# Performance work log

Hardware: AMD Instinct MI355X
Metric: run time of the kernel (lower is better)

The kernel has to match this reference:

```python
import jax, jax.numpy as jnp
import numpy as np

# dims matching init_kwargs
B, N = 1, 2048
VOCAB, DIM, DEPTH = 32000, 1024, 4
HEADS, DIM_HEAD, WINDOW = 16, 64, 512
INNER = HEADS * DIM_HEAD          # 1024
FF_INNER = int(DIM * 4 * 2 / 3)   # 2730 (GEGLU inner)
DPB_DIM = DIM // 2
LN_EPS = 1e-5


def layernorm(x, g, b):
    m = jnp.mean(x, axis=-1, keepdims=True)
    v = jnp.mean(jnp.square(x - m), axis=-1, keepdims=True)
    return (x - m) * jax.lax.rsqrt(v + LN_EPS) * g + b


def look_around(x, backward=1, forward=0, pad_value=-1):
    # x: [b, nw, w, ...]; concat shifted windows along the window_size axis
    nw = x.shape[1]
    pads = [(0, 0), (backward, forward)] + [(0, 0)] * (x.ndim - 2)
    px = jnp.pad(x, pads, constant_values=pad_value)
    return jnp.concatenate([px[:, i:i + nw] for i in range(backward + forward + 1)], axis=2)


def dynamic_pos_bias(w1, b1, w2, b2, w3, b3, i, j):
    # MLP over scalar relative distances, then gather into [H, i, j]
    rel = jnp.arange(j, dtype=jnp.float32)[:, None]            # [j, 1]
    h = jax.nn.silu(rel @ w1 + b1)
    h = jax.nn.silu(h @ w2 + b2)
    bias = h @ w3 + b3                                          # [j, H]
    idx = jnp.abs(jnp.arange(j - i, j)[:, None] - jnp.arange(j)[None, :])  # [i, j]
    return jnp.transpose(bias[idx], (2, 0, 1))                  # [H, i, j]


def local_attention(q, k, v, attn_bias):
    # causal sliding-window attention, look_backward=1, look_forward=0, exact_windowsize=True
    # q,k,v: [B,H,N,dh]; N assumed multiple of WINDOW (autopad is a no-op then)
    b, h, n, d = q.shape
    w = WINDOW
    nw = n // w
    scale = d ** -0.5
    bq = q.reshape(b * h, nw, w, d) * scale
    bk = look_around(k.reshape(b * h, nw, w, d), pad_value=-1.0)   # [bh,nw,2w,d]
    bv = look_around(v.reshape(b * h, nw, w, d), pad_value=-1.0)
    t = jnp.arange(n).reshape(1, nw, w)
    bq_t = t[..., :, None]                                      # [1,nw,w,1]
    bq_k = look_around(t, pad_value=-1)[..., None, :]           # [1,nw,1,2w]
    # causal | exact-window | padding masks
    mask = (bq_t < bq_k) | (bq_t > bq_k + w) | (bq_k == -1)
    sim = jnp.einsum('bwid,bwjd->bwij', bq, bk)                 # [bh,nw,w,2w]
    sim = (sim.reshape(b, h, nw, w, 2 * w) + attn_bias[None, :, None]).reshape(b * h, nw, w, 2 * w)
    sim = jnp.where(mask, -jnp.finfo(sim.dtype).max, sim)
    attn = jax.nn.softmax(sim, axis=-1)
    out = jnp.einsum('bwij,bwjd->bwid', attn, bv)
    return out.reshape(b, h, n, d)


def forward(tokens, tok_emb, pos_emb, dpb_w1, dpb_b1, dpb_w2, dpb_b2, dpb_w3, dpb_b3,
            ln1_g, ln1_b, Wqkv, Wo, ln2_g, ln2_b, Wff1, Wff2, lnf_g, lnf_b, Wlogits):
    bsz, n = tokens.shape
    x = tok_emb[tokens] + pos_emb[:n]                           # [B,N,D]
    bias = dynamic_pos_bias(dpb_w1, dpb_b1, dpb_w2, dpb_b2, dpb_w3, dpb_b3, WINDOW, 2 * WINDOW)

    def split_heads(t):
        return t.reshape(bsz, n, HEADS, DIM_HEAD).transpose(0, 2, 1, 3)

    for l in range(DEPTH):
        # LocalMHA (prenorm) + residual
        h = layernorm(x, ln1_g[l], ln1_b[l])
        q, k, v = jnp.split(h @ Wqkv[l], 3, axis=-1)
        o = local_attention(split_heads(q), split_heads(k), split_heads(v), bias)
        o = o.transpose(0, 2, 1, 3).reshape(bsz, n, INNER)
        x = x + o @ Wo[l]
        # GEGLU FFN (prenorm inside FeedForward) + residual
        h = layernorm(x, ln2_g[l], ln2_b[l])
        a, gate = jnp.split(h @ Wff1[l], 2, axis=-1)
        x = x + (a * jax.nn.gelu(gate, approximate=False)) @ Wff2[l]

    return layernorm(x, lnf_g, lnf_b) @ Wlogits                 # [B,N,V]


def setup_inputs() -> dict:
    key = jax.random.key(0)
    ks = iter(jax.random.split(key, 16))
    s = 0.02
    rn = lambda *shape: jax.random.normal(next(ks), shape, dtype=jnp.float32) * s
    return {
        'tokens': jax.random.randint(next(ks), (B, N), 0, VOCAB, dtype=jnp.int32),
        'tok_emb': rn(VOCAB, DIM),
        'pos_emb': rn(N, DIM),
        'dpb_w1': rn(1, DPB_DIM), 'dpb_b1': jnp.zeros((DPB_DIM,), jnp.float32),
        'dpb_w2': rn(DPB_DIM, DPB_DIM), 'dpb_b2': jnp.zeros((DPB_DIM,), jnp.float32),
        'dpb_w3': rn(DPB_DIM, HEADS), 'dpb_b3': jnp.zeros((HEADS,), jnp.float32),
        'ln1_g': jnp.ones((DEPTH, DIM), jnp.float32), 'ln1_b': jnp.zeros((DEPTH, DIM), jnp.float32),
        'Wqkv': rn(DEPTH, DIM, 3 * INNER),
        'Wo': rn(DEPTH, INNER, DIM),
        'ln2_g': jnp.ones((DEPTH, DIM), jnp.float32), 'ln2_b': jnp.zeros((DEPTH, DIM), jnp.float32),
        'Wff1': rn(DEPTH, DIM, 2 * FF_INNER),
        'Wff2': rn(DEPTH, FF_INNER, DIM),
        'lnf_g': jnp.ones((DIM,), jnp.float32), 'lnf_b': jnp.zeros((DIM,), jnp.float32),
        'Wlogits': rn(DIM, VOCAB),
    }


def reference(tokens, tok_emb, pos_emb, dpb_w1, dpb_b1, dpb_w2, dpb_b2, dpb_w3, dpb_b3,
              ln1_g, ln1_b, Wqkv, Wo, ln2_g, ln2_b, Wff1, Wff2, lnf_g, lnf_b, Wlogits):
    return forward(tokens, tok_emb, pos_emb, dpb_w1, dpb_b1, dpb_w2, dpb_b2, dpb_w3, dpb_b3,
                   ln1_g, ln1_b, Wqkv, Wo, ln2_g, ln2_b, Wff1, Wff2, lnf_g, lnf_b, Wlogits)
```

## Files before the change

### kernel.cpp

```cpp
#include <hip/hip_runtime.h>
#include <cstdint>

#define DEV __device__ __forceinline__

typedef __attribute__((ext_vector_type(8))) short bf16x8;
typedef __attribute__((ext_vector_type(4))) short bf16x4;
typedef __attribute__((ext_vector_type(4))) float f32x4;
typedef __attribute__((ext_vector_type(8))) unsigned short u16x8;

DEV float bf2f(unsigned short u) { return __uint_as_float(((unsigned)u) << 16); }
DEV unsigned short f2bf(float f) {
  unsigned u = __float_as_uint(f);
  u += 0x7FFFu + ((u >> 16) & 1u);
  return (unsigned short)(u >> 16);
}

DEV void gload_lds16(const void* g, void* lds) {
  __builtin_amdgcn_global_load_lds(
      (const __attribute__((address_space(1))) unsigned int*)g,
      (__attribute__((address_space(3))) unsigned int*)lds, 16, 0, 0);
}

__global__ __launch_bounds__(256) void k_prep(
    const int* __restrict__ tokens, const float* __restrict__ tok_emb,
    const float* __restrict__ pos_emb, float* __restrict__ x,
    const float* __restrict__ w1, const float* __restrict__ b1,
    const float* __restrict__ w2, const float* __restrict__ b2,
    const float* __restrict__ w3, const float* __restrict__ b3,
    float* __restrict__ table,
    const float* __restrict__ Wqkv, unsigned short* __restrict__ WqkvT,
    const float* __restrict__ Wo, unsigned short* __restrict__ WoT,
    const float* __restrict__ Wff1, unsigned short* __restrict__ Wff1T,
    const float* __restrict__ Wff2, unsigned short* __restrict__ Wff2T,
    const float* __restrict__ Wlog, unsigned short* __restrict__ WlogT) {
  __shared__ float smem[64 * 65];
  int b = blockIdx.x, t = threadIdx.x;
  if (b < 2048) {
    int tok = tokens[b];
    int c = t * 4;
    float4 a = *(const float4*)(tok_emb + (long)tok * 1024 + c);
    float4 p = *(const float4*)(pos_emb + (long)b * 1024 + c);
    float4 r;
    r.x = a.x + p.x; r.y = a.y + p.y; r.z = a.z + p.z; r.w = a.w + p.w;
    *(float4*)(x + (long)b * 1024 + c) = r;
    return;
  }
  b -= 2048;
  if (b < 1024) {
    float* h1 = smem;
    float* h2 = smem + 512;
    float rf = (float)b;
    for (int c = t; c < 512; c += 256) {
      float v = rf * w1[c] + b1[c];
      h1[c] = v / (1.0f + __expf(-v));
    }
    __syncthreads();
    for (int c = t; c < 512; c += 256) {
      float acc = b2[c];
      for (int k2 = 0; k2 < 512; ++k2) acc = fmaf(h1[k2], w2[(long)k2 * 512 + c], acc);
      h2[c] = acc / (1.0f + __expf(-acc));
    }
    __syncthreads();
    if (t < 16) {
      float acc = b3[t];
      for (int k2 = 0; k2 < 512; ++k2) acc = fmaf(h2[k2], w3[k2 * 16 + t], acc);
      table[b * 16 + t] = acc;
    }
    return;
  }
  b -= 1024;
  const float* src; unsigned short* dst;
  int K, N, Kp, nx, ny, mode;
  long ss, ds;
  if (b < 3072) {
    src = Wqkv; dst = WqkvT; K = 1024; N = 3072; Kp = 1024;
    nx = 48; ny = 16; mode = 0; ss = 1024L * 3072; ds = 3072L * 1024;
  } else if ((b -= 3072) < 1024) {
    src = Wo; dst = WoT; K = 1024; N = 1024; Kp = 1024;
    nx = 16; ny = 16; mode = 0; ss = 1024L * 1024; ds = 1024L * 1024;
  } else if ((b -= 1024) < 5504) {
    src = Wff1; dst = Wff1T; K = 1024; N = 5460; Kp = 1024;
    nx = 86; ny = 16; mode = 1; ss = 1024L * 5460; ds = 5504L * 1024;
  } else if ((b -= 5504) < 2752) {
    src = Wff2; dst = Wff2T; K = 2730; N = 1024; Kp = 2752;
    nx = 16; ny = 43; mode = 0; ss = 2730L * 1024; ds = 1024L * 2752;
  } else {
    b -= 2752;
    src = Wlog; dst = WlogT; K = 1024; N = 32000; Kp = 1024;
    nx = 500; ny = 16; mode = 0; ss = 0; ds = 0;
  }
  int z = b / (nx * ny);
  int rem = b % (nx * ny);
  int n0 = (rem % nx) * 64, k0 = (rem / nx) * 64;
  src += (long)z * ss;
  dst += (long)z * ds;
  float (*tile)[65] = (float(*)[65])smem;
  const int cr = t >> 4, cc = (t & 15) * 4;
#pragma unroll
  for (int i = 0; i < 4; ++i) {
    int kr = cr + 16 * i;
    int k = k0 + kr, n = n0 + cc;
    float4 v = make_float4(0.f, 0.f, 0.f, 0.f);
    if (k < K && n < N) v = *(const float4*)(src + (long)k * N + n);
    tile[kr][cc + 0] = v.x;
    tile[kr][cc + 1] = v.y;
    tile[kr][cc + 2] = v.z;
    tile[kr][cc + 3] = v.w;
  }
  __syncthreads();
  const int kc = (t & 7) * 8;
#pragma unroll
  for (int it = 0; it < 2; ++it) {
    int nr = (t >> 3) + 32 * it;
    u16x8 o;
#pragma unroll
    for (int e = 0; e < 8; ++e) o[e] = f2bf(tile[kc + e][nr]);
    int nrow = n0 + nr;
    if (mode)
      nrow = nrow < 2730 ? 2 * nrow : (nrow < 5460 ? 2 * (nrow - 2730) + 1 : nrow);
    *(u16x8*)(dst + (long)nrow * Kp + k0 + kc) = o;
  }
}

__global__ __launch_bounds__(256) void k_ln4(const float* __restrict__ x,
    const float* __restrict__ g, const float* __restrict__ b,
    unsigned short* __restrict__ out) {
  const int row = blockIdx.x * 4 + (threadIdx.x >> 6);
  const int l = threadIdx.x & 63;
  const float* xr = x + (long)row * 1024 + l * 16;
  float4 v[4];
#pragma unroll
  for (int e = 0; e < 4; ++e) v[e] = ((const float4*)xr)[e];
  float s = 0.0f;
#pragma unroll
  for (int e = 0; e < 4; ++e) s += v[e].x + v[e].y + v[e].z + v[e].w;
#pragma unroll
  for (int off = 32; off; off >>= 1) s += __shfl_xor(s, off);
  float mean = s * (1.0f / 1024.0f);
  float sq = 0.0f;
#pragma unroll
  for (int e = 0; e < 4; ++e) {
    float a0 = v[e].x - mean, a1 = v[e].y - mean, a2 = v[e].z - mean, a3 = v[e].w - mean;
    sq += a0 * a0 + a1 * a1 + a2 * a2 + a3 * a3;
  }
#pragma unroll
  for (int off = 32; off; off >>= 1) sq += __shfl_xor(sq, off);
  float inv = rsqrtf(sq * (1.0f / 1024.0f) + 1e-5f);
  const float* gr = g + l * 16;
  const float* br = b + l * 16;
  unsigned short* orow = out + (long)row * 1024 + l * 16;
#pragma unroll
  for (int e = 0; e < 4; ++e) {
    float4 gv = ((const float4*)gr)[e];
    float4 bv = ((const float4*)br)[e];
    ushort4 o;
    o.x = f2bf((v[e].x - mean) * inv * gv.x + bv.x);
    o.y = f2bf((v[e].y - mean) * inv * gv.y + bv.y);
    o.z = f2bf((v[e].z - mean) * inv * gv.z + bv.z);
    o.w = f2bf((v[e].w - mean) * inv * gv.w + bv.w);
    ((ushort4*)orow)[e] = o;
  }
}

__global__ __launch_bounds__(256, 2) void k_attn_mfma(
    const unsigned short* __restrict__ qkv, const float* __restrict__ table,
    unsigned short* __restrict__ o) {
  __shared__ unsigned short Ks[64 * 64];
  __shared__ unsigned short Vt[64 * 72];
  __shared__ unsigned short Ps[4][16 * 72];
  __shared__ float biasl[1024];
  const int qt = blockIdx.x, h = blockIdx.y, wi = blockIdx.z;
  const int iw0 = qt * 64;
  const int t = threadIdx.x;
  const int w = t >> 6, l = t & 63;
  const int lq = l & 15, lk = l >> 4;

  for (int i = t; i < 1024; i += 256) biasl[i] = table[i * 16 + h];

  const unsigned short* qp = qkv + (long)(wi * 512 + iw0 + w * 16 + lq) * 3072 + h * 64;
  bf16x8 qf0 = *(const bf16x8*)(qp + lk * 8);
  bf16x8 qf1 = *(const bf16x8*)(qp + 32 + lk * 8);

  f32x4 oacc[4] = {};
  float mrun[4] = {-3.0e38f, -3.0e38f, -3.0e38f, -3.0e38f};
  float srun[4] = {};

  const int kt0 = (wi == 0) ? 8 : qt;
  const int kt1 = qt + 8;
  for (int kt = kt0; kt <= kt1; ++kt) {
    const int ktbase = kt * 64;
    const long kgbase = (long)((wi - 1) * 512 + ktbase);
    __syncthreads();
    {
      const unsigned short* Kg = qkv + kgbase * 3072 + 1024 + h * 64;
#pragma unroll
      for (int s2 = 0; s2 < 2; ++s2) {
        int g = s2 * 4 + w;
        int row = g * 8 + (l >> 3);
        int gch = (l & 7) ^ (row & 7);
        gload_lds16(Kg + (long)row * 3072 + gch * 8, &Ks[g * 512]);
      }
    }
    {
      int kp = t & 31, dg = t >> 5;
      const unsigned short* Vg =
          qkv + (kgbase + 2 * kp) * 3072 + 2048 + h * 64 + dg * 8;
      bf16x8 a0 = *(const bf16x8*)Vg;
      bf16x8 a1 = *(const bf16x8*)(Vg + 3072);
#pragma unroll
      for (int e = 0; e < 8; ++e) {
        unsigned pack = ((unsigned)(unsigned short)a0[e]) |
                        (((unsigned)(unsigned short)a1[e]) << 16);
        *(unsigned*)&Vt[(dg * 8 + e) * 72 + 2 * kp] = pack;
      }
    }
    asm volatile("s_waitcnt vmcnt(0)" ::: "memory");
    __syncthreads();

    f32x4 sacc[4] = {};
#pragma unroll
    for (int ct = 0; ct < 4; ++ct) {
      int krow = ct * 16 + lq;
      bf16x8 kf0 = *(const bf16x8*)&Ks[krow * 64 + (((0 + lk) ^ (krow & 7)) * 8)];
      bf16x8 kf1 = *(const bf16x8*)&Ks[krow * 64 + (((4 + lk) ^ (krow & 7)) * 8)];
      sacc[ct] = __builtin_amdgcn_mfma_f32_16x16x32_bf16(qf0, kf0, sacc[ct], 0, 0, 0);
      sacc[ct] = __builtin_amdgcn_mfma_f32_16x16x32_bf16(qf1, kf1, sacc[ct], 0, 0, 0);
    }

#pragma unroll
    for (int r = 0; r < 4; ++r) {
      const int iw = iw0 + w * 16 + lk * 4 + r;
      float sc[4];
#pragma unroll
      for (int ct = 0; ct < 4; ++ct) {
        int jj = ktbase + ct * 16 + lq;
        int di = 512 + iw - jj;
        int dic = min(max(di, 0), 1023);
        bool allowed = (jj >= iw) && (jj <= iw + 512);
        float v = sacc[ct][r] * 0.125f + biasl[dic];
        sc[ct] = allowed ? v : -3.0e38f;
      }
      float mx = fmaxf(fmaxf(sc[0], sc[1]), fmaxf(sc[2], sc[3]));
      mx = fmaxf(mx, __shfl_xor(mx, 1));
      mx = fmaxf(mx, __shfl_xor(mx, 2));
      mx = fmaxf(mx, __shfl_xor(mx, 4));
      mx = fmaxf(mx, __shfl_xor(mx, 8));
      float mnew = fmaxf(mrun[r], mx);
      float f = __expf(mrun[r] - mnew);
      mrun[r] = mnew;
      float rs = 0.0f;
#pragma unroll
      for (int ct = 0; ct < 4; ++ct) {
        float pv = __expf(sc[ct] - mnew);
        rs += pv;
        Ps[w][(lk * 4 + r) * 72 + ct * 16 + lq] = f2bf(pv);
      }
      rs += __shfl_xor(rs, 1);
      rs += __shfl_xor(rs, 2);
      rs += __shfl_xor(rs, 4);
      rs += __shfl_xor(rs, 8);
      srun[r] = srun[r] * f + rs;
#pragma unroll
      for (int dt = 0; dt < 4; ++dt) oacc[dt][r] *= f;
    }
    asm volatile("s_waitcnt lgkmcnt(0)" ::: "memory");

#pragma unroll
    for (int ks = 0; ks < 2; ++ks) {
      bf16x4 pa0 = *(const bf16x4*)&Ps[w][lq * 72 + ks * 32 + lk * 8];
      bf16x4 pa1 = *(const bf16x4*)&Ps[w][lq * 72 + ks * 32 + lk * 8 + 4];
      bf16x8 pa = __builtin_shufflevector(pa0, pa1, 0, 1, 2, 3, 4, 5, 6, 7);
#pragma unroll
      for (int dt = 0; dt < 4; ++dt) {
        int drow = dt * 16 + lq;
        bf16x4 vb0 = *(const bf16x4*)&Vt[drow * 72 + ks * 32 + lk * 8];
        bf16x4 vb1 = *(const bf16x4*)&Vt[drow * 72 + ks * 32 + lk * 8 + 4];
        bf16x8 vb = __builtin_shufflevector(vb0, vb1, 0, 1, 2, 3, 4, 5, 6, 7);
        oacc[dt] = __builtin_amdgcn_mfma_f32_16x16x32_bf16(pa, vb, oacc[dt], 0, 0, 0);
      }
    }
  }

  unsigned short* ob =
      o + (long)(wi * 512 + iw0 + w * 16 + lk * 4) * 1024 + h * 64 + lq;
#pragma unroll
  for (int r = 0; r < 4; ++r) {
    float inv = 1.0f / srun[r];
#pragma unroll
    for (int dt = 0; dt < 4; ++dt)
      ob[(long)r * 1024 + dt * 16] = f2bf(oacc[dt][r] * inv);
  }
}

template <int EPI, int BM>
__global__ __launch_bounds__(256, 2) void k_gemm(const unsigned short* __restrict__ A,
    const unsigned short* __restrict__ BT, void* __restrict__ Cout,
    int N, int K, int nbm) {
  constexpr int MI = BM / 32;
  __shared__ unsigned short As[BM * 64];
  __shared__ unsigned short Bs[128 * 64];
  const int nwg = gridDim.x;
  const int orig = blockIdx.x;
  const int q8 = nwg >> 3, r8 = nwg & 7;
  const int xcd = orig & 7, i8 = orig >> 3;
  const int wgid = (xcd < r8 ? xcd * (q8 + 1) : r8 * (q8 + 1) + (xcd - r8) * q8) + i8;
  const int bm = wgid % nbm;
  const int bn = wgid / nbm;
  const int t = threadIdx.x;
  const int w = t >> 6, l = t & 63;
  const int wm = w >> 1, wn = w & 1;
  const int lrow = l >> 3, lch = l & 7;
  const int lq = l & 15, lk = l >> 4;
  f32x4 acc[MI][4] = {};
  const long arow0 = (long)bm * BM, brow0 = (long)bn * 128;
  for (int kt = 0; kt < K; kt += 64) {
    __syncthreads();
#pragma unroll
    for (int s2 = 0; s2 < 4; ++s2) {
      int grp = s2 * 4 + w;
      int r = grp * 8 + lrow;
      int gch = lch ^ lrow;
      gload_lds16(BT + (brow0 + r) * K + kt + gch * 8, &Bs[grp * 512]);
      if (s2 < MI)
        gload_lds16(A + (arow0 + r) * K + kt + gch * 8, &As[grp * 512]);
    }
    asm volatile("s_waitcnt vmcnt(0)" ::: "memory");
    __syncthreads();
#pragma unroll
    for (int kk = 0; kk < 2; ++kk) {
      bf16x8 af[MI], bfr[4];
#pragma unroll
      for (int i = 0; i < MI; ++i) {
        int ra = wm * (BM / 2) + i * 16 + lq;
        af[i] = *(const bf16x8*)&As[ra * 64 + (((kk * 4 + lk) ^ (ra & 7)) * 8)];
      }
#pragma unroll
      for (int j = 0; j < 4; ++j) {
        int rb = wn * 64 + j * 16 + lq;
        bfr[j] = *(const bf16x8*)&Bs[rb * 64 + (((kk * 4 + lk) ^ (rb & 7)) * 8)];
      }
#pragma unroll
      for (int i = 0; i < MI; ++i)
#pragma unroll
        for (int j = 0; j < 4; ++j)
          acc[i][j] = __builtin_amdgcn_mfma_f32_16x16x32_bf16(af[i], bfr[j],
                                                              acc[i][j], 0, 0, 0);
    }
  }
  const int rbase = bm * BM + wm * (BM / 2) + lk * 4;
  const int cbase = bn * 128 + wn * 64 + lq;
#pragma unroll
  for (int i = 0; i < MI; ++i) {
#pragma unroll
    for (int j = 0; j < 4; ++j) {
#pragma unroll
      for (int r2 = 0; r2 < 4; ++r2) {
        long row = rbase + i * 16 + r2;
        long col = cbase + j * 16;
        float v = acc[i][j][r2];
        if (EPI == 0) {
          ((unsigned short*)Cout)[row * N + col] = f2bf(v);
        } else if (EPI == 1) {
          ((float*)Cout)[row * N + col] += v;
        } else if (EPI == 2) {
          ((float*)Cout)[row * N + col] = v;
        } else {
          float gpart = __shfl_xor(v, 1);
          if ((lq & 1) == 0) {
            float uval =
                v * (0.5f * gpart * (1.0f + erff(gpart * 0.70710678118654752f)));
            ((unsigned short*)Cout)[row * (N >> 1) + (col >> 1)] = f2bf(uval);
          }
        }
      }
    }
  }
}

extern "C" void kernel_launch(void* const* d_in, const int* in_sizes, int n_in,
                              void* d_out, int out_size, void* d_ws, size_t ws_size,
                              hipStream_t stream) {
  (void)in_sizes; (void)n_in; (void)out_size; (void)ws_size;
  const int* tokens   = (const int*)d_in[0];
  const float* tok_emb = (const float*)d_in[1];
  const float* pos_emb = (const float*)d_in[2];
  const float* dpb_w1 = (const float*)d_in[3];
  const float* dpb_b1 = (const float*)d_in[4];
  const float* dpb_w2 = (const float*)d_in[5];
  const float* dpb_b2 = (const float*)d_in[6];
  const float* dpb_w3 = (const float*)d_in[7];
  const float* dpb_b3 = (const float*)d_in[8];
  const float* ln1_g  = (const float*)d_in[9];
  const float* ln1_b  = (const float*)d_in[10];
  const float* Wqkv   = (const float*)d_in[11];
  const float* Wo     = (const float*)d_in[12];
  const float* ln2_g  = (const float*)d_in[13];
  const float* ln2_b  = (const float*)d_in[14];
  const float* Wff1   = (const float*)d_in[15];
  const float* Wff2   = (const float*)d_in[16];
  const float* lnf_g  = (const float*)d_in[17];
  const float* lnf_b  = (const float*)d_in[18];
  const float* Wlog   = (const float*)d_in[19];
  float* out = (float*)d_out;

  char* p = (char*)d_ws;
  auto carve = [&](size_t bytes) {
    char* q = p;
    p += (bytes + 255) & ~(size_t)255;
    return (void*)q;
  };
  unsigned short* WqkvT = (unsigned short*)carve((size_t)4 * 3072 * 1024 * 2);
  unsigned short* WoT   = (unsigned short*)carve((size_t)4 * 1024 * 1024 * 2);
  unsigned short* Wff1T = (unsigned short*)carve((size_t)4 * 5504 * 1024 * 2);
  unsigned short* Wff2T = (unsigned short*)carve((size_t)4 * 1024 * 2752 * 2);
  unsigned short* WlogT = (unsigned short*)carve((size_t)32000 * 1024 * 2);
  float*          x     = (float*)carve((size_t)2048 * 1024 * 4);
  unsigned short* hbuf  = (unsigned short*)carve((size_t)2048 * 1024 * 2);
  unsigned short* qkv   = (unsigned short*)carve((size_t)2048 * 3072 * 2);
  unsigned short* ao    = (unsigned short*)carve((size_t)2048 * 1024 * 2);
  unsigned short* ubuf  = (unsigned short*)carve((size_t)2048 * 2752 * 2);
  float*          table = (float*)carve((size_t)1024 * 16 * 4);

  k_prep<<<23424, 256, 0, stream>>>(
      tokens, tok_emb, pos_emb, x, dpb_w1, dpb_b1, dpb_w2, dpb_b2, dpb_w3,
      dpb_b3, table, Wqkv, WqkvT, Wo, WoT, Wff1, Wff1T, Wff2, Wff2T, Wlog, WlogT);

  for (int l = 0; l < 4; ++l) {
    k_ln4<<<512, 256, 0, stream>>>(x, ln1_g + l * 1024, ln1_b + l * 1024, hbuf);
    k_gemm<0, 128><<<dim3(16 * (3072 / 128)), 256, 0, stream>>>(
        hbuf, WqkvT + (long)l * 3072 * 1024, qkv, 3072, 1024, 16);
    k_attn_mfma<<<dim3(8, 16, 4), 256, 0, stream>>>(qkv, table, ao);
    k_gemm<1, 64><<<dim3(32 * (1024 / 128)), 256, 0, stream>>>(
        ao, WoT + (long)l * 1024 * 1024, x, 1024, 1024, 32);
    k_ln4<<<512, 256, 0, stream>>>(x, ln2_g + l * 1024, ln2_b + l * 1024, hbuf);
    k_gemm<3, 128><<<dim3(16 * (5504 / 128)), 256, 0, stream>>>(
        hbuf, Wff1T + (long)l * 5504 * 1024, ubuf, 5504, 1024, 16);
    k_gemm<1, 64><<<dim3(32 * (1024 / 128)), 256, 0, stream>>>(
        ubuf, Wff2T + (long)l * 1024 * 2752, x, 1024, 2752, 32);
  }
  k_ln4<<<512, 256, 0, stream>>>(x, lnf_g, lnf_b, hbuf);
  k_gemm<2, 128><<<dim3(16 * (32000 / 128)), 256, 0, stream>>>(
      hbuf, WlogT, out, 32000, 1024, 16);
}
```

Baseline: 1.047 ms.

## Pre-tile weights into swizzled 128x64 blocks so GEMM B-loads are contiguous

The weight conversion kernel now writes each transposed bf16 weight as contiguous 128-row by 64-k tiles, already XOR-swizzled to match the LDS layout. The GEMM B-operand load then becomes one linear 16-byte-per-lane copy per tile, with no per-row strided addressing. Prep blocks now cover 128x64 tiles, which halves the prep grid, and the GEGLU interleave is handled by a separate gather path. The cost is a more complex prep kernel with a larger shared tile, plus reliance on every GEMM N being a multiple of 128.

Result: slower. 1.072 ms (+2.4%).

```diff
diff --git a/kernel.cpp b/kernel.cpp
--- a/kernel.cpp
+++ b/kernel.cpp
@@ -33,7 +33,7 @@
     const float* __restrict__ Wff1, unsigned short* __restrict__ Wff1T,
     const float* __restrict__ Wff2, unsigned short* __restrict__ Wff2T,
     const float* __restrict__ Wlog, unsigned short* __restrict__ WlogT) {
-  __shared__ float smem[64 * 65];
+  __shared__ float smem[64 * 132];
   int b = blockIdx.x, t = threadIdx.x;
   if (b < 2048) {
     int tok = tokens[b];
@@ -70,55 +70,100 @@
   }
   b -= 1024;
   const float* src; unsigned short* dst;
-  int K, N, Kp, nx, ny, mode;
-  long ss, ds;
-  if (b < 3072) {
-    src = Wqkv; dst = WqkvT; K = 1024; N = 3072; Kp = 1024;
-    nx = 48; ny = 16; mode = 0; ss = 1024L * 3072; ds = 3072L * 1024;
-  } else if ((b -= 3072) < 1024) {
-    src = Wo; dst = WoT; K = 1024; N = 1024; Kp = 1024;
-    nx = 16; ny = 16; mode = 0; ss = 1024L * 1024; ds = 1024L * 1024;
-  } else if ((b -= 1024) < 5504) {
-    src = Wff1; dst = Wff1T; K = 1024; N = 5460; Kp = 1024;
-    nx = 86; ny = 16; mode = 1; ss = 1024L * 5460; ds = 5504L * 1024;
-  } else if ((b -= 5504) < 2752) {
-    src = Wff2; dst = Wff2T; K = 2730; N = 1024; Kp = 2752;
-    nx = 16; ny = 43; mode = 0; ss = 2730L * 1024; ds = 1024L * 2752;
+  int N, Kreal, nt, kt, mode;
+  if (b < 1536) {
+    int z = b / 384, r = b % 384;
+    nt = r / 16; kt = r % 16; mode = 0; N = 3072; Kreal = 1024;
+    src = Wqkv + (long)z * 1024 * 3072;
+    dst = WqkvT + ((long)z * 384 + r) * 8192;
+  } else if ((b -= 1536) < 512) {
+    int z = b / 128, r = b % 128;
+    nt = r / 16; kt = r % 16; mode = 0; N = 1024; Kreal = 1024;
+    src = Wo + (long)z * 1024 * 1024;
+    dst = WoT + ((long)z * 128 + r) * 8192;
+  } else if ((b -= 512) < 2752) {
+    int z = b / 688, r = b % 688;
+    nt = r / 16; kt = r % 16; mode = 1; N = 5460; Kreal = 1024;
+    src = Wff1 + (long)z * 1024 * 5460;
+    dst = Wff1T + ((long)z * 688 + r) * 8192;
+  } else if ((b -= 2752) < 1376) {
+    int z = b / 344, r = b % 344;
+    nt = r / 43; kt = r % 43; mode = 0; N = 1024; Kreal = 2730;
+    src = Wff2 + (long)z * 2730 * 1024;
+    dst = Wff2T + ((long)z * 344 + r) * 8192;
   } else {
-    b -= 2752;
-    src = Wlog; dst = WlogT; K = 1024; N = 32000; Kp = 1024;
-    nx = 500; ny = 16; mode = 0; ss = 0; ds = 0;
-  }
-  int z = b / (nx * ny);
-  int rem = b % (nx * ny);
-  int n0 = (rem % nx) * 64, k0 = (rem / nx) * 64;
-  src += (long)z * ss;
-  dst += (long)z * ds;
-  float (*tile)[65] = (float(*)[65])smem;
-  const int cr = t >> 4, cc = (t & 15) * 4;
-#pragma unroll
-  for (int i = 0; i < 4; ++i) {
-    int kr = cr + 16 * i;
-    int k = k0 + kr, n = n0 + cc;
-    float4 v = make_float4(0.f, 0.f, 0.f, 0.f);
-    if (k < K && n < N) v = *(const float4*)(src + (long)k * N + n);
-    tile[kr][cc + 0] = v.x;
-    tile[kr][cc + 1] = v.y;
-    tile[kr][cc + 2] = v.z;
-    tile[kr][cc + 3] = v.w;
+    b -= 1376;
+    nt = b / 16; kt = b % 16; mode = 0; N = 32000; Kreal = 1024;
+    src = Wlog;
+    dst = WlogT + (long)b * 8192;
+  }
+  const int k0 = kt * 64;
+  float (*tf)[132] = (float(*)[132])smem;
+  if (mode == 0) {
+    const int nb = nt * 128 + (t & 15) * 8;
+#pragma unroll
+    for (int ii = 0; ii < 4; ++ii) {
+      int row = (t >> 4) + 16 * ii;
+      int k = k0 + row;
+      float4 v0 = {0.f, 0.f, 0.f, 0.f}, v1 = v0;
+      if (k < Kreal) {
+        const float* sp = src + (long)k * N + nb;
+        v0 = *(const float4*)sp;
+        v1 = *(const float4*)(sp + 4);
+      }
+      int cs = (t & 15) * 8;
+      *(float4*)&tf[row][cs] = v0;
+      *(float4*)&tf[row][cs + 4] = v1;
+    }
+  } else {
+    const int row = t >> 2;
+    const int k = k0 + row;
+    const int fo = (t & 3) * 16;
+    const int fb = nt * 64;
+    const float* sr = src + (long)k * 5460;
+#pragma unroll
+    for (int j = 0; j < 4; ++j) {
+      int f = fb + fo + 4 * j;
+      float4 av;
+      if (f + 3 < 2730) {
+        av = *(const float4*)(sr + f);
+      } else {
+        av.x = (f < 2730) ? sr[f] : 0.f;
+        av.y = (f + 1 < 2730) ? sr[f + 1] : 0.f;
+        av.z = (f + 2 < 2730) ? sr[f + 2] : 0.f;
+        av.w = 0.f;
+      }
+      int lc = 2 * (fo + 4 * j);
+      tf[row][lc + 0] = av.x;
+      tf[row][lc + 2] = av.y;
+      tf[row][lc + 4] = av.z;
+      tf[row][lc + 6] = av.w;
+    }
+#pragma unroll
+    for (int j = 0; j < 8; ++j) {
+      int f = fb + fo + 2 * j;
+      float2 gv;
+      if (f + 1 < 2730) {
+        gv = *(const float2*)(sr + 2730 + f);
+      } else {
+        gv.x = (f < 2730) ? sr[2730 + f] : 0.f;
+        gv.y = 0.f;
+      }
+      int lc = 2 * (fo + 2 * j) + 1;
+      tf[row][lc] = gv.x;
+      tf[row][lc + 2] = gv.y;
+    }
   }
   __syncthreads();
-  const int kc = (t & 7) * 8;
-#pragma unroll
-  for (int it = 0; it < 2; ++it) {
-    int nr = (t >> 3) + 32 * it;
+  const int r = t & 127;
+  const int c8b = (t >> 7) * 4;
+#pragma unroll
+  for (int cc = 0; cc < 4; ++cc) {
+    int c8 = c8b + cc;
     u16x8 o;
 #pragma unroll
-    for (int e = 0; e < 8; ++e) o[e] = f2bf(tile[kc + e][nr]);
-    int nrow = n0 + nr;
-    if (mode)
-      nrow = nrow < 2730 ? 2 * nrow : (nrow < 5460 ? 2 * (nrow - 2730) + 1 : nrow);
-    *(u16x8*)(dst + (long)nrow * Kp + k0 + kc) = o;
+    for (int e = 0; e < 8; ++e) o[e] = f2bf(tf[c8 * 8 + e][r]);
+    *(u16x8*)(dst + r * 64 + ((c8 ^ (r & 7)) * 8)) = o;
   }
 }
 
@@ -294,7 +339,7 @@
 
 template <int EPI, int BM>
 __global__ __launch_bounds__(256, 2) void k_gemm(const unsigned short* __restrict__ A,
-    const unsigned short* __restrict__ BT, void* __restrict__ Cout,
+    const unsigned short* __restrict__ BTt, void* __restrict__ Cout,
     int N, int K, int nbm) {
   constexpr int MI = BM / 32;
   __shared__ unsigned short As[BM * 64];
@@ -312,17 +357,20 @@
   const int lrow = l >> 3, lch = l & 7;
   const int lq = l & 15, lk = l >> 4;
   f32x4 acc[MI][4] = {};
-  const long arow0 = (long)bm * BM, brow0 = (long)bn * 128;
+  const long arow0 = (long)bm * BM;
+  const unsigned short* btile = BTt + (long)bn * (K >> 6) * 8192;
   for (int kt = 0; kt < K; kt += 64) {
     __syncthreads();
+    const unsigned short* bsrc = btile + (long)(kt >> 6) * 8192 + l * 8;
 #pragma unroll
     for (int s2 = 0; s2 < 4; ++s2) {
       int grp = s2 * 4 + w;
-      int r = grp * 8 + lrow;
-      int gch = lch ^ lrow;
-      gload_lds16(BT + (brow0 + r) * K + kt + gch * 8, &Bs[grp * 512]);
-      if (s2 < MI)
+      gload_lds16(bsrc + grp * 512, &Bs[grp * 512]);
+      if (s2 < MI) {
+        int r = grp * 8 + lrow;
+        int gch = lch ^ lrow;
         gload_lds16(A + (arow0 + r) * K + kt + gch * 8, &As[grp * 512]);
+      }
     }
     asm volatile("s_waitcnt vmcnt(0)" ::: "memory");
     __syncthreads();
@@ -421,7 +469,7 @@
   unsigned short* ubuf  = (unsigned short*)carve((size_t)2048 * 2752 * 2);
   float*          table = (float*)carve((size_t)1024 * 16 * 4);
 
-  k_prep<<<23424, 256, 0, stream>>>(
+  k_prep<<<13248, 256, 0, stream>>>(
       tokens, tok_emb, pos_emb, x, dpb_w1, dpb_b1, dpb_w2, dpb_b2, dpb_w3,
       dpb_b3, table, Wqkv, WqkvT, Wo, WoT, Wff1, Wff1T, Wff2, Wff2T, Wlog, WlogT);
 
```
